# Kernel tuning notes

Measured on AMD Instinct MI355X. Metric: run time of the kernel, lower is better.

## Reference

```python
import jax, jax.numpy as jnp
import numpy as np
from jax import lax

CH, GROUP = 32, 8  # channel=32, subchannel=4 -> group=8

def conv2d(x, w, b, pad):
    # x: [B,C,H,W], w: [O,I,kh,kw]
    out = lax.conv_general_dilated(x, w, (1, 1), [(pad, pad), (pad, pad)],
                                   dimension_numbers=("NCHW", "OIHW", "NCHW"))
    return out + b[None, :, None, None]

def pconv(x, w, b):
    # 1x1 conv as einsum; w: [O,I]
    return jnp.einsum("oi,bihw->bohw", w, x) + b[None, :, None, None]

def setup_inputs() -> dict:
    key = jax.random.key(0)
    ks = jax.random.split(key, 32)
    s = 0.05
    d = {
        "x": jax.random.normal(ks[0], (8, CH, 64, 64), jnp.float32),
        "y": jax.random.normal(ks[1], (8, 1, 64, 64), jnp.float32),
        "conv_w": jax.random.normal(ks[2], (CH, CH + GROUP, 3, 3), jnp.float32) * s,
        "conv_b": jax.random.normal(ks[3], (CH,), jnp.float32) * s,
        "score_w": jax.random.normal(ks[4], (1, CH, 3, 3), jnp.float32) * s,
        "score_b": jax.random.normal(ks[5], (1,), jnp.float32) * s,
        "c132_w": jax.random.normal(ks[6], (32, 1, 3, 3), jnp.float32) * s,
        "c132_b": jax.random.normal(ks[7], (32,), jnp.float32) * s,
        "q1_w": jax.random.normal(ks[8], (32, 32), jnp.float32) * s,
        "q1_b": jax.random.normal(ks[9], (32,), jnp.float32) * s,
        "k1_w": jax.random.normal(ks[10], (32, 32), jnp.float32) * s,
        "k1_b": jax.random.normal(ks[11], (32,), jnp.float32) * s,
        "q2_w": jax.random.normal(ks[12], (32, 32), jnp.float32) * s,
        "q2_b": jax.random.normal(ks[13], (32,), jnp.float32) * s,
        "k2_w": jax.random.normal(ks[14], (32, 32), jnp.float32) * s,
        "k2_b": jax.random.normal(ks[15], (32,), jnp.float32) * s,
        "q3_w": jax.random.normal(ks[16], (32, 32), jnp.float32) * s,
        "q3_b": jax.random.normal(ks[17], (32,), jnp.float32) * s,
        "k3_w": jax.random.normal(ks[18], (32, 32), jnp.float32) * s,
        "k3_b": jax.random.normal(ks[19], (32,), jnp.float32) * s,
        "conv6_w": jax.random.normal(ks[20], (32, 64), jnp.float32) * s,
        "conv6_b": jax.random.normal(ks[21], (32,), jnp.float32) * s,
    }
    return d

def reference(x, y, conv_w, conv_b, score_w, score_b, c132_w, c132_b,
              q1_w, q1_b, k1_w, k1_b, q2_w, q2_b, k2_w, k2_b,
              q3_w, q3_b, k3_w, k3_b, conv6_w, conv6_b):
    B, C, H, W = x.shape
    sub = C // GROUP
    # group-wise chunk + interleave y: [x_g0, y, x_g1, y, ...]
    xg = x.reshape(B, GROUP, sub, H, W)
    yb = jnp.broadcast_to(y[:, None], (B, GROUP, 1, H, W))
    x_cat = jnp.concatenate([xg, yb], axis=2).reshape(B, C + GROUP, H, W)
    x1_co = jax.nn.relu(conv2d(x_cat, conv_w, conv_b, 1))        # [B,32,H,W]
    x2_co = conv2d(y, c132_w, c132_b, 1)                          # [B,32,H,W]

    HW = H * W
    x_query1 = pconv(x1_co, q1_w, q1_b).reshape(B, 32, HW)
    x_key1 = pconv(x1_co, k1_w, k1_b).reshape(B, 32, HW)
    x_query2 = pconv(x1_co, q2_w, q2_b).reshape(B, 32, HW)
    x_key2 = pconv(x1_co, k2_w, k2_b).reshape(B, 32, HW)
    y_query = pconv(x2_co, q3_w, q3_b).reshape(B, 32, HW)
    y_key = pconv(x2_co, k3_w, k3_b).reshape(B, 32, HW)

    # spatial attention [B, HW, HW]
    x_hw = jax.nn.softmax(jnp.einsum("bcn,bcm->bnm", x_query1, x_key2), axis=-1)
    # channel attention [B, 32, 32]
    x_c = jax.nn.softmax(jnp.einsum("bcn,bdn->bcd", x_key1, x_query2), axis=-1)

    xy_hw = jnp.einsum("bcn,bnm->bcm", y_query, x_hw).reshape(B, 32, H, W)
    xy_c = jnp.einsum("bcd,bcn->bdn", x_c, y_key).reshape(B, 32, H, W)

    out_final = pconv(jnp.concatenate([xy_hw, xy_c], axis=1), conv6_w, conv6_b)
    x_out = x + out_final
    y_out = y + conv2d(x_out, score_w, score_b, 1)
    return (x_out, y_out)
```

## Files before the change

kernel.cpp:

```cpp
#include <hip/hip_runtime.h>
#include <hip/hip_bf16.h>
#include <math.h>

#define HW 4096

typedef short bf16x8_t __attribute__((ext_vector_type(8)));
typedef float f32x16_t __attribute__((ext_vector_type(16)));
typedef unsigned int u32;
typedef unsigned int u32x4_t __attribute__((ext_vector_type(4)));
typedef int i32x2_t __attribute__((ext_vector_type(2)));

union castu { u32x4_t u; bf16x8_t s; };

static __device__ __forceinline__ unsigned short f2bf(float f){
    union { __bf16 b; unsigned short u; } c; c.b = (__bf16)f; return c.u;
}
static __device__ __forceinline__ u32 pk2(float lo, float hi){
    return ((u32)f2bf(hi) << 16) | (u32)f2bf(lo);
}
static __device__ __forceinline__ bf16x8_t ldb(const unsigned short* p){
    return *reinterpret_cast<const bf16x8_t*>(p);
}
static __device__ __forceinline__ bf16x8_t ld_xs(const unsigned short* p){
    uint2 lo = *(const uint2*)(p);
    uint2 hi = *(const uint2*)(p + 4);
    castu c; c.u = (u32x4_t){lo.x, lo.y, hi.x, hi.y};
    return c.s;
}
static __device__ __forceinline__ f32x16_t mfma32(bf16x8_t a, bf16x8_t b, f32x16_t c){
    return __builtin_amdgcn_mfma_f32_32x32x16_bf16(a, b, c, 0, 0, 0);
}

#define EXP2_MAG  8388608.0f
#define EXP2_BIAS 1064986816.0f

static __device__ __forceinline__ float fexp2(float x){
    return __int_as_float((int)fmaf(x, EXP2_MAG, EXP2_BIAS));
}
static __device__ __forceinline__ u32 pkexp2(float lo, float hi){
    u32 i0 = (u32)(int)fmaf(lo, EXP2_MAG, EXP2_BIAS);
    u32 i1 = (u32)(int)fmaf(hi, EXP2_MAG, EXP2_BIAS);
#if __has_builtin(__builtin_amdgcn_perm)
    return __builtin_amdgcn_perm(i1, i0, 0x07060302u);
#else
    return (i1 & 0xFFFF0000u) | (i0 >> 16);
#endif
}

static __device__ __forceinline__ void cd2bfrag(const u32 P[8], bf16x8_t& b0, bf16x8_t& b1){
    i32x2_t s02 = __builtin_amdgcn_permlane32_swap((int)P[0], (int)P[2], false, false);
    i32x2_t s13 = __builtin_amdgcn_permlane32_swap((int)P[1], (int)P[3], false, false);
    i32x2_t s46 = __builtin_amdgcn_permlane32_swap((int)P[4], (int)P[6], false, false);
    i32x2_t s57 = __builtin_amdgcn_permlane32_swap((int)P[5], (int)P[7], false, false);
    castu c0, c1;
    c0.u = (u32x4_t){ (u32)s02[0], (u32)s13[0], (u32)s02[1], (u32)s13[1] };
    c1.u = (u32x4_t){ (u32)s46[0], (u32)s57[0], (u32)s46[1], (u32)s57[1] };
    b0 = c0.s; b1 = c1.s;
}

#define LOG2E 1.44269504088896340736f


__global__ __launch_bounds__(256, 1) void k_front_mfma(
    const float* __restrict__ x, const float* __restrict__ y,
    const float* __restrict__ conv_w, const float* __restrict__ conv_b,
    const float* __restrict__ c132_w, const float* __restrict__ c132_b,
    const float* __restrict__ q1w, const float* __restrict__ q1b,
    const float* __restrict__ k1w, const float* __restrict__ k1b,
    const float* __restrict__ q2w, const float* __restrict__ q2b,
    const float* __restrict__ k2w, const float* __restrict__ k2b,
    const float* __restrict__ q3w, const float* __restrict__ q3b,
    const float* __restrict__ k3w, const float* __restrict__ k3b,
    float* __restrict__ K1, float* __restrict__ Q2, float* __restrict__ YQ,
    unsigned short* __restrict__ Q1t, unsigned short* __restrict__ K2t,
    unsigned short* __restrict__ YKt)
{
    __shared__ unsigned short xs[4 * 68 * 36];
    __shared__ float ys[4 * 68];
    __shared__ u32 wplane[18 * 4 * 64];
    __shared__ u32 wyplane[4 * 64];
    __shared__ u32 c1plane[4 * 64];

    int tid = threadIdx.x;
    int h0 = blockIdx.x * 2, b = blockIdx.y;

    #pragma unroll
    for (int i = 0; i < 32; ++i){
        int idx = i * 256 + tid;
        int w = idx & 63, ic = (idx >> 6) & 31, dr = idx >> 11;
        int hr = h0 - 1 + dr;
        float v = (hr >= 0 && hr < 64) ? x[((b * 32 + ic) << 12) + (hr << 6) + w] : 0.f;
        xs[(dr * 68 + w + 1) * 36 + ic] = f2bf(v);
    }
    {
        int dr = tid >> 6, ic = tid & 31, side = (tid >> 5) & 1;
        xs[(dr * 68 + (side ? 65 : 0)) * 36 + ic] = 0;
    }
    for (int idx = tid; idx < 272; idx += 256){
        int dr = idx / 68, wp = idx % 68;
        int hr = h0 - 1 + dr, w = wp - 1;
        ys[idx] = (hr >= 0 && hr < 64 && w >= 0 && w < 64) ? y[(b << 12) + (hr << 6) + w] : 0.f;
    }
    for (int e = tid; e < 4608; e += 256){
        int f = e >> 8, wi = (e >> 6) & 3, ln = e & 63;
        int t = f >> 1, j = f & 1, hh = ln >> 5, ll = ln & 31;
        int ic0 = 16 * j + 8 * hh + 2 * wi;
        int co0 = 5 * (ic0 >> 2) + (ic0 & 3);
        int ic1 = ic0 + 1;
        int co1 = 5 * (ic1 >> 2) + (ic1 & 3);
        wplane[e] = pk2(conv_w[ll * 360 + co0 * 9 + t], conv_w[ll * 360 + co1 * 9 + t]);
    }
    {
        int wi = tid >> 6, ln = tid & 63, hh = ln >> 5, ll = ln & 31;
        u32 vy = 0, vc = 0;
        if (hh == 0){
            int t0 = 2 * wi, t1 = 2 * wi + 1;
            float s0 = 0.f, s1 = 0.f;
            #pragma unroll
            for (int g = 0; g < 8; ++g){
                s0 += conv_w[ll * 360 + (5 * g + 4) * 9 + t0];
                s1 += conv_w[ll * 360 + (5 * g + 4) * 9 + t1];
            }
            vy = pk2(s0, s1);
            vc = pk2(c132_w[ll * 9 + t0], c132_w[ll * 9 + t1]);
        } else if (wi == 0){
            float s0 = 0.f;
            #pragma unroll
            for (int g = 0; g < 8; ++g) s0 += conv_w[ll * 360 + (5 * g + 4) * 9 + 8];
            vy = pk2(s0, 0.f);
            vc = pk2(c132_w[ll * 9 + 8], 0.f);
        }
        wyplane[wi * 64 + ln] = vy;
        c1plane[wi * 64 + ln] = vc;
    }
    __syncthreads();

    int lane = tid & 63, wid = tid >> 6;
    int l31 = lane & 31, h = lane >> 5;
    int wr = wid >> 1, toff = (wid & 1) * 32;
    int wpB = toff + l31;

    bf16x8_t wA[18];
    #pragma unroll
    for (int f = 0; f < 18; ++f){
        castu c;
        c.u = (u32x4_t){ wplane[(f * 4 + 0) * 64 + lane], wplane[(f * 4 + 1) * 64 + lane],
                         wplane[(f * 4 + 2) * 64 + lane], wplane[(f * 4 + 3) * 64 + lane] };
        wA[f] = c.s;
    }
    castu wyf, c1f;
    wyf.u = (u32x4_t){ wyplane[lane], wyplane[64 + lane], wyplane[128 + lane], wyplane[192 + lane] };
    c1f.u = (u32x4_t){ c1plane[lane], c1plane[64 + lane], c1plane[128 + lane], c1plane[192 + lane] };

    float yv[8];
    #pragma unroll
    for (int i = 0; i < 8; ++i){
        int tt = 8 * h + i;
        yv[i] = (tt < 9) ? ys[(wr + tt / 3) * 68 + wpB + (tt % 3)] : 0.f;
    }
    castu yf;
    yf.u = (u32x4_t){ pk2(yv[0], yv[1]), pk2(yv[2], yv[3]), pk2(yv[4], yv[5]), pk2(yv[6], yv[7]) };

    f32x16_t accE, accO, accY, acc2;
    #pragma unroll
    for (int r = 0; r < 16; ++r){
        int oc = (r & 3) + 8 * (r >> 2) + 4 * h;
        accE[r] = 0.f; accO[r] = 0.f;
        accY[r] = conv_b[oc]; acc2[r] = c132_b[oc];
    }
    #pragma unroll
    for (int t = 0; t < 9; ++t){
        int base = ((wr + t / 3) * 68 + wpB + (t % 3)) * 36 + 8 * h;
        bf16x8_t b0 = ld_xs(xs + base);
        bf16x8_t b1 = ld_xs(xs + base + 16);
        if (t & 1){
            accO = mfma32(wA[t * 2 + 0], b0, accO);
            accO = mfma32(wA[t * 2 + 1], b1, accO);
        } else {
            accE = mfma32(wA[t * 2 + 0], b0, accE);
            accE = mfma32(wA[t * 2 + 1], b1, accE);
        }
    }
    accY = mfma32(wyf.s, yf.s, accY);
    acc2 = mfma32(c1f.s, yf.s, acc2);

    f32x16_t x1v;
    #pragma unroll
    for (int r = 0; r < 16; ++r){
        float v = accE[r] + accO[r] + accY[r];
        x1v[r] = v > 0.f ? v : 0.f;
    }
    u32 P[8];
    bf16x8_t x1b0, x1b1, x2b0, x2b1;
    #pragma unroll
    for (int t2 = 0; t2 < 8; ++t2) P[t2] = pk2(x1v[2 * t2], x1v[2 * t2 + 1]);
    cd2bfrag(P, x1b0, x1b1);
    #pragma unroll
    for (int t2 = 0; t2 < 8; ++t2) P[t2] = pk2(acc2[2 * t2], acc2[2 * t2 + 1]);
    cd2bfrag(P, x2b0, x2b1);

    int pxg = (h0 + wr) * 64 + toff + l31;
    int tile = ((h0 + wr) << 1) + (wid & 1);
    size_t tb = ((size_t)b * 128 + tile) * 1024;

    {
        f32x16_t a;
        #pragma unroll
        for (int r = 0; r < 16; ++r) a[r] = q1b[(r & 3) + 8 * (r >> 2) + 4 * h];
        const float* p0 = q1w + l31 * 32 + 8 * h;
        castu w0, w1;
        w0.u = (u32x4_t){ pk2(p0[0],p0[1]), pk2(p0[2],p0[3]), pk2(p0[4],p0[5]), pk2(p0[6],p0[7]) };
        w1.u = (u32x4_t){ pk2(p0[16],p0[17]), pk2(p0[18],p0[19]), pk2(p0[20],p0[21]), pk2(p0[22],p0[23]) };
        a = mfma32(w0.s, x1b0, a);
        a = mfma32(w1.s, x1b1, a);
        u32 Q[8];
        #pragma unroll
        for (int t2 = 0; t2 < 8; ++t2) Q[t2] = pk2(a[2 * t2] * LOG2E, a[2 * t2 + 1] * LOG2E);
        bf16x8_t f0, f1; cd2bfrag(Q, f0, f1);
        *(bf16x8_t*)(Q1t + tb + lane * 8)       = f0;
        *(bf16x8_t*)(Q1t + tb + 512 + lane * 8) = f1;
    }
    {
        f32x16_t a;
        #pragma unroll
        for (int r = 0; r < 16; ++r) a[r] = k1b[(r & 3) + 8 * (r >> 2) + 4 * h];
        const float* p0 = k1w + l31 * 32 + 8 * h;
        castu w0, w1;
        w0.u = (u32x4_t){ pk2(p0[0],p0[1]), pk2(p0[2],p0[3]), pk2(p0[4],p0[5]), pk2(p0[6],p0[7]) };
        w1.u = (u32x4_t){ pk2(p0[16],p0[17]), pk2(p0[18],p0[19]), pk2(p0[20],p0[21]), pk2(p0[22],p0[23]) };
        a = mfma32(w0.s, x1b0, a);
        a = mfma32(w1.s, x1b1, a);
        #pragma unroll
        for (int r = 0; r < 16; ++r)
            K1[(b * 32 + (r & 3) + 8 * (r >> 2) + 4 * h) * HW + pxg] = a[r];
    }
    {
        f32x16_t a;
        #pragma unroll
        for (int r = 0; r < 16; ++r) a[r] = q2b[(r & 3) + 8 * (r >> 2) + 4 * h];
        const float* p0 = q2w + l31 * 32 + 8 * h;
        castu w0, w1;
        w0.u = (u32x4_t){ pk2(p0[0],p0[1]), pk2(p0[2],p0[3]), pk2(p0[4],p0[5]), pk2(p0[6],p0[7]) };
        w1.u = (u32x4_t){ pk2(p0[16],p0[17]), pk2(p0[18],p0[19]), pk2(p0[20],p0[21]), pk2(p0[22],p0[23]) };
        a = mfma32(w0.s, x1b0, a);
        a = mfma32(w1.s, x1b1, a);
        #pragma unroll
        for (int r = 0; r < 16; ++r)
            Q2[(b * 32 + (r & 3) + 8 * (r >> 2) + 4 * h) * HW + pxg] = a[r];
    }
    {
        f32x16_t a;
        #pragma unroll
        for (int r = 0; r < 16; ++r) a[r] = k2b[(r & 3) + 8 * (r >> 2) + 4 * h];
        const float* p0 = k2w + l31 * 32 + 8 * h;
        castu w0, w1;
        w0.u = (u32x4_t){ pk2(p0[0],p0[1]), pk2(p0[2],p0[3]), pk2(p0[4],p0[5]), pk2(p0[6],p0[7]) };
        w1.u = (u32x4_t){ pk2(p0[16],p0[17]), pk2(p0[18],p0[19]), pk2(p0[20],p0[21]), pk2(p0[22],p0[23]) };
        a = mfma32(w0.s, x1b0, a);
        a = mfma32(w1.s, x1b1, a);
        u32 Q[8];
        #pragma unroll
        for (int t2 = 0; t2 < 8; ++t2) Q[t2] = pk2(a[2 * t2], a[2 * t2 + 1]);
        bf16x8_t f0, f1; cd2bfrag(Q, f0, f1);
        *(bf16x8_t*)(K2t + tb + lane * 8)       = f0;
        *(bf16x8_t*)(K2t + tb + 512 + lane * 8) = f1;
    }
    {
        f32x16_t a;
        #pragma unroll
        for (int r = 0; r < 16; ++r) a[r] = q3b[(r & 3) + 8 * (r >> 2) + 4 * h];
        const float* p0 = q3w + l31 * 32 + 8 * h;
        castu w0, w1;
        w0.u = (u32x4_t){ pk2(p0[0],p0[1]), pk2(p0[2],p0[3]), pk2(p0[4],p0[5]), pk2(p0[6],p0[7]) };
        w1.u = (u32x4_t){ pk2(p0[16],p0[17]), pk2(p0[18],p0[19]), pk2(p0[20],p0[21]), pk2(p0[22],p0[23]) };
        a = mfma32(w0.s, x2b0, a);
        a = mfma32(w1.s, x2b1, a);
        #pragma unroll
        for (int r = 0; r < 16; ++r)
            YQ[(b * 32 + (r & 3) + 8 * (r >> 2) + 4 * h) * HW + pxg] = a[r];
    }
    {
        f32x16_t a;
        #pragma unroll
        for (int r = 0; r < 16; ++r) a[r] = k3b[(r & 3) + 8 * (r >> 2) + 4 * h];
        const float* p0 = k3w + l31 * 32 + 8 * h;
        castu w0, w1;
        w0.u = (u32x4_t){ pk2(p0[0],p0[1]), pk2(p0[2],p0[3]), pk2(p0[4],p0[5]), pk2(p0[6],p0[7]) };
        w1.u = (u32x4_t){ pk2(p0[16],p0[17]), pk2(p0[18],p0[19]), pk2(p0[20],p0[21]), pk2(p0[22],p0[23]) };
        a = mfma32(w0.s, x2b0, a);
        a = mfma32(w1.s, x2b1, a);
        u32 Q[8];
        #pragma unroll
        for (int t2 = 0; t2 < 8; ++t2) Q[t2] = pk2(a[2 * t2], a[2 * t2 + 1]);
        bf16x8_t f0, f1; cd2bfrag(Q, f0, f1);
        *(bf16x8_t*)(YKt + tb + lane * 8)       = f0;
        *(bf16x8_t*)(YKt + tb + 512 + lane * 8) = f1;
    }
}

__global__ __launch_bounds__(256) void k_chan_part(
    const float* __restrict__ K1, const float* __restrict__ Q2,
    float* __restrict__ Scp)
{
    __shared__ float k1s[128 * 33];
    __shared__ float q2s[128 * 33];
    int b = blockIdx.x & 7;
    int chunk = blockIdx.x >> 3;
    int n0 = chunk * 128;
    int t = threadIdx.x;
    for (int i = 0; i < 16; ++i){
        int idx = i * 256 + t;
        int c = idx >> 7, nl = idx & 127;
        k1s[nl * 33 + c] = K1[(b * 32 + c) * HW + n0 + nl];
        q2s[nl * 33 + c] = Q2[(b * 32 + c) * HW + n0 + nl];
    }
    __syncthreads();
    float acc[4] = {0.f, 0.f, 0.f, 0.f};
    int d = t & 31, c0 = t >> 5;
    for (int nl = 0; nl < 128; ++nl){
        float qv = q2s[nl * 33 + d];
        #pragma unroll
        for (int i = 0; i < 4; ++i)
            acc[i] = fmaf(k1s[nl * 33 + c0 + 8 * i], qv, acc[i]);
    }
    #pragma unroll
    for (int i = 0; i < 4; ++i)
        Scp[(b * 32 + chunk) * 1024 + (c0 + 8 * i) * 32 + d] = acc[i];
}

__global__ __launch_bounds__(1024) void k_chan_fin(
    const float* __restrict__ Scp, const float* __restrict__ c6w,
    float* __restrict__ M2)
{
    __shared__ float pc[32 * 33];
    int b = blockIdx.x;
    int t = threadIdx.x;
    int c = t >> 5, d = t & 31;
    float s = 0.f;
    for (int k = 0; k < 32; ++k) s += Scp[(b * 32 + k) * 1024 + t];
    float mx = s;
    #pragma unroll
    for (int off = 16; off >= 1; off >>= 1) mx = fmaxf(mx, __shfl_xor(mx, off));
    float e = __expf(s - mx);
    float sum = e;
    #pragma unroll
    for (int off = 16; off >= 1; off >>= 1) sum += __shfl_xor(sum, off);
    pc[c * 33 + d] = e / sum;
    __syncthreads();
    int o = t >> 5, cc = t & 31;
    float m2 = 0.f;
    #pragma unroll
    for (int dd = 0; dd < 32; ++dd)
        m2 = fmaf(c6w[o * 64 + 32 + dd], pc[cc * 33 + dd], m2);
    M2[b * 1024 + o * 32 + cc] = m2;
}

__global__ __launch_bounds__(256, 4) void k_stats_mfma(
    const unsigned short* __restrict__ Q1t, const unsigned short* __restrict__ K2t,
    const float* __restrict__ YQ, unsigned short* __restrict__ YQ2)
{
    __shared__ float red[4][16][64];
    __shared__ float ls[32];
    int t = threadIdx.x, wid = t >> 6, lane = t & 63;
    int l31 = lane & 31, h = lane >> 5;
    int b = blockIdx.x & 7, ntile = blockIdx.x >> 3;
    int n0 = ntile * 32;
    size_t qtb = ((size_t)b * 128 + ntile) * 1024;
    bf16x8_t a0 = ldb(Q1t + qtb + lane * 8);
    bf16x8_t a1 = ldb(Q1t + qtb + 512 + lane * 8);
    float accl[16];
    #pragma unroll
    for (int r = 0; r < 16; ++r) accl[r] = 0.f;

    const unsigned short* kp = K2t + ((size_t)b * 128 + (wid << 5)) * 1024 + lane * 8;
    bf16x8_t b0 = ldb(kp), b1 = ldb(kp + 512);
    f32x16_t s_cur;
    #pragma unroll
    for (int r = 0; r < 16; ++r) s_cur[r] = 0.f;
    s_cur = mfma32(a0, b0, s_cur);
    s_cur = mfma32(a1, b1, s_cur);
    kp += 1024;
    bf16x8_t b0n = ldb(kp), b1n = ldb(kp + 512);

    #pragma unroll 4
    for (int i = 0; i < 32; ++i){
        f32x16_t s_nxt;
        #pragma unroll
        for (int r = 0; r < 16; ++r) s_nxt[r] = 0.f;
        __builtin_amdgcn_s_setprio(1);
        s_nxt = mfma32(a0, b0n, s_nxt);
        s_nxt = mfma32(a1, b1n, s_nxt);
        __builtin_amdgcn_s_setprio(0);
        kp += (i < 30) ? 1024 : 0;
        bf16x8_t b0nn = ldb(kp), b1nn = ldb(kp + 512);
        #pragma unroll
        for (int r = 0; r < 16; ++r) accl[r] += fexp2(s_cur[r]);
        s_cur = s_nxt; b0n = b0nn; b1n = b1nn;
    }
    #pragma unroll
    for (int r = 0; r < 16; ++r) red[wid][r][lane] = accl[r];
    __syncthreads();
    if (wid == 0){
        #pragma unroll
        for (int r = 0; r < 16; ++r){
            float v = red[0][r][lane] + red[1][r][lane] + red[2][r][lane] + red[3][r][lane];
            #pragma unroll
            for (int off = 16; off >= 1; off >>= 1) v += __shfl_xor(v, off);
            if (l31 == 0)
                ls[(r & 3) + 8 * (r >> 2) + 4 * h] = 1.0f / v;
        }
    }
    __syncthreads();
    size_t otb = ((size_t)b * 128 + ntile) * 1024;
    #pragma unroll
    for (int p = 0; p < 4; ++p){
        int idx = (p << 8) + t;
        int c = idx >> 5, n = idx & 31;
        size_t g = (size_t)(b * 32 + c) * HW + n0 + n;
        int j = n >> 4, hh = (n >> 3) & 1;
        YQ2[otb + j * 512 + (c + (hh << 5)) * 8 + (n & 7)] = f2bf(YQ[g] * ls[n]);
    }
}

__global__ __launch_bounds__(256, 4) void k_attn_mfma(
    const unsigned short* __restrict__ Q1t, const unsigned short* __restrict__ K2t,
    const unsigned short* __restrict__ YKt, const unsigned short* __restrict__ YQ2,
    const float* __restrict__ M2, const float* __restrict__ c6w, const float* __restrict__ c6b,
    const float* __restrict__ x, float* __restrict__ xout)
{
    __shared__ float red[4][16][64];
    int t = threadIdx.x, wid = t >> 6, lane = t & 63;
    int l31 = lane & 31, h = lane >> 5;
    int b = blockIdx.x & 7, mtile = blockIdx.x >> 3;
    int m0 = mtile * 32;
    size_t ktb = ((size_t)b * 128 + mtile) * 1024;

    bf16x8_t kb0 = ldb(K2t + ktb + lane * 8);
    bf16x8_t kb1 = ldb(K2t + ktb + 512 + lane * 8);

    f32x16_t oacc;
    #pragma unroll
    for (int r = 0; r < 16; ++r) oacc[r] = 0.f;

    const unsigned short* qp = Q1t + ((size_t)b * 128 + (wid << 5)) * 1024 + lane * 8;
    const unsigned short* yp = YQ2 + ((size_t)b * 128 + (wid << 5)) * 1024 + lane * 8;

    bf16x8_t a0 = ldb(qp), a1 = ldb(qp + 512);
    bf16x8_t y0 = ldb(yp), y1 = ldb(yp + 512);
    f32x16_t s_cur;
    #pragma unroll
    for (int r = 0; r < 16; ++r) s_cur[r] = 0.f;
    s_cur = mfma32(a0, kb0, s_cur);
    s_cur = mfma32(a1, kb1, s_cur);
    qp += 1024; yp += 1024;
    bf16x8_t a0n = ldb(qp), a1n = ldb(qp + 512);
    bf16x8_t y0n = ldb(yp), y1n = ldb(yp + 512);

    #pragma unroll 4
    for (int i = 0; i < 32; ++i){
        f32x16_t s_nxt;
        #pragma unroll
        for (int r = 0; r < 16; ++r) s_nxt[r] = 0.f;
        __builtin_amdgcn_s_setprio(1);
        s_nxt = mfma32(a0n, kb0, s_nxt);
        s_nxt = mfma32(a1n, kb1, s_nxt);
        __builtin_amdgcn_s_setprio(0);
        int adv = (i < 30) ? 1024 : 0;
        qp += adv; yp += adv;
        bf16x8_t a0nn = ldb(qp), a1nn = ldb(qp + 512);
        bf16x8_t y0nn = ldb(yp), y1nn = ldb(yp + 512);
        u32 P[8];
        #pragma unroll
        for (int tt = 0; tt < 8; ++tt)
            P[tt] = pkexp2(s_cur[2 * tt], s_cur[2 * tt + 1]);
        bf16x8_t e0, e1;
        cd2bfrag(P, e0, e1);
        __builtin_amdgcn_s_setprio(1);
        oacc = mfma32(y0, e0, oacc);
        oacc = mfma32(y1, e1, oacc);
        __builtin_amdgcn_s_setprio(0);
        s_cur = s_nxt;
        a0n = a0nn; a1n = a1nn;
        y0 = y0n; y1 = y1n; y0n = y0nn; y1n = y1nn;
    }
    #pragma unroll
    for (int r = 0; r < 16; ++r) red[wid][r][lane] = oacc[r];
    __syncthreads();
    if (wid != 0) return;
    #pragma unroll
    for (int r = 0; r < 16; ++r)
        oacc[r] = red[0][r][lane] + red[1][r][lane] + red[2][r][lane] + red[3][r][lane];

    u32 P[8];
    #pragma unroll
    for (int tt = 0; tt < 8; ++tt) P[tt] = pk2(oacc[2 * tt], oacc[2 * tt + 1]);
    bf16x8_t xb0, xb1;
    cd2bfrag(P, xb0, xb1);

    const float* w1p = c6w + l31 * 64;
    const float* m2p = M2 + b * 1024 + l31 * 32;
    int cb0 = 8 * h, cb1 = 16 + 8 * h;
    castu wa0, wa1, ma0, ma1;
    wa0.u = (u32x4_t){ pk2(w1p[cb0], w1p[cb0+1]), pk2(w1p[cb0+2], w1p[cb0+3]),
                       pk2(w1p[cb0+4], w1p[cb0+5]), pk2(w1p[cb0+6], w1p[cb0+7]) };
    wa1.u = (u32x4_t){ pk2(w1p[cb1], w1p[cb1+1]), pk2(w1p[cb1+2], w1p[cb1+3]),
                       pk2(w1p[cb1+4], w1p[cb1+5]), pk2(w1p[cb1+6], w1p[cb1+7]) };
    ma0.u = (u32x4_t){ pk2(m2p[cb0], m2p[cb0+1]), pk2(m2p[cb0+2], m2p[cb0+3]),
                       pk2(m2p[cb0+4], m2p[cb0+5]), pk2(m2p[cb0+6], m2p[cb0+7]) };
    ma1.u = (u32x4_t){ pk2(m2p[cb1], m2p[cb1+1]), pk2(m2p[cb1+2], m2p[cb1+3]),
                       pk2(m2p[cb1+4], m2p[cb1+5]), pk2(m2p[cb1+6], m2p[cb1+7]) };
    bf16x8_t ykb0 = ldb(YKt + ktb + lane * 8);
    bf16x8_t ykb1 = ldb(YKt + ktb + 512 + lane * 8);

    f32x16_t facc;
    #pragma unroll
    for (int r = 0; r < 16; ++r) facc[r] = c6b[(r & 3) + 8 * (r >> 2) + 4 * h];
    facc = mfma32(wa0.s, xb0, facc);
    facc = mfma32(wa1.s, xb1, facc);
    facc = mfma32(ma0.s, ykb0, facc);
    facc = mfma32(ma1.s, ykb1, facc);

    #pragma unroll
    for (int r = 0; r < 16; ++r){
        int o = (r & 3) + 8 * (r >> 2) + 4 * h;
        size_t gi = ((size_t)(b * 32 + o) << 12) + m0 + l31;
        xout[gi] = x[gi] + facc[r];
    }
}

__global__ __launch_bounds__(256) void k_score(
    const float* __restrict__ xout, const float* __restrict__ y,
    const float* __restrict__ sw, const float* __restrict__ sb,
    float* __restrict__ yout)
{
    __shared__ float xs[3][32][66];
    __shared__ float red[4][64];
    int tid = threadIdx.x;
    int b = blockIdx.x & 7, h = blockIdx.x >> 3;
    for (int i = 0; i < 24; ++i){
        int idx = i * 256 + tid;
        int w = idx & 63, ic = (idx >> 6) & 31, dr = idx >> 11;
        int hr = h + dr - 1;
        xs[dr][ic][1 + w] = (hr >= 0 && hr < 64) ? xout[((b * 32 + ic) << 12) + (hr << 6) + w] : 0.f;
    }
    if (tid < 96){ xs[tid >> 5][tid & 31][0] = 0.f; }
    else if (tid < 192){ int u = tid - 96; xs[u >> 5][u & 31][65] = 0.f; }
    __syncthreads();
    int w = tid & 63, icg = tid >> 6;
    float p = 0.f;
    #pragma unroll
    for (int i = 0; i < 8; ++i){
        int ic = icg * 8 + i;
        #pragma unroll
        for (int tap = 0; tap < 9; ++tap)
            p = fmaf(sw[ic * 9 + tap], xs[tap / 3][ic][w + tap % 3], p);
    }
    red[icg][w] = p;
    __syncthreads();
    if (tid < 64){
        int px = (h << 6) + tid;
        yout[b * HW + px] = y[b * HW + px] + sb[0]
                          + red[0][tid] + red[1][tid] + red[2][tid] + red[3][tid];
    }
}

extern "C" void kernel_launch(void* const* d_in, const int* in_sizes, int n_in,
                              void* d_out, int out_size, void* d_ws, size_t ws_size,
                              hipStream_t stream)
{
    (void)in_sizes; (void)n_in; (void)out_size; (void)ws_size;
    const float* x      = (const float*)d_in[0];
    const float* y      = (const float*)d_in[1];
    const float* conv_w = (const float*)d_in[2];
    const float* conv_b = (const float*)d_in[3];
    const float* score_w= (const float*)d_in[4];
    const float* score_b= (const float*)d_in[5];
    const float* c132_w = (const float*)d_in[6];
    const float* c132_b = (const float*)d_in[7];
    const float* q1w = (const float*)d_in[8];  const float* q1b = (const float*)d_in[9];
    const float* k1w = (const float*)d_in[10]; const float* k1b = (const float*)d_in[11];
    const float* q2w = (const float*)d_in[12]; const float* q2b = (const float*)d_in[13];
    const float* k2w = (const float*)d_in[14]; const float* k2b = (const float*)d_in[15];
    const float* q3w = (const float*)d_in[16]; const float* q3b = (const float*)d_in[17];
    const float* k3w = (const float*)d_in[18]; const float* k3b = (const float*)d_in[19];
    const float* c6w = (const float*)d_in[20]; const float* c6b = (const float*)d_in[21];

    float* ws = (float*)d_ws;
    const size_t SZ = 1048576;
    float* Scp = ws;
    float* M2  = ws + 262144;
    float* K1  = ws + 2 * SZ;
    float* Q2  = ws + 3 * SZ;
    float* YQf = ws + 4 * SZ;
    unsigned short* Q1t = (unsigned short*)(ws + 5 * SZ);
    unsigned short* K2t = (unsigned short*)(ws + 5 * SZ + SZ / 2);
    unsigned short* YKt = (unsigned short*)(ws + 6 * SZ);
    unsigned short* YQ2 = (unsigned short*)(ws + 6 * SZ + SZ / 2);

    float* xout = (float*)d_out;
    float* yout = xout + SZ;

    k_front_mfma<<<dim3(32, 8), 256, 0, stream>>>(
        x, y, conv_w, conv_b, c132_w, c132_b,
        q1w, q1b, k1w, k1b, q2w, q2b, k2w, k2b, q3w, q3b, k3w, k3b,
        K1, Q2, YQf, Q1t, K2t, YKt);
    k_chan_part<<<256, 256, 0, stream>>>(K1, Q2, Scp);
    k_chan_fin<<<8, 1024, 0, stream>>>(Scp, c6w, M2);
    k_stats_mfma<<<1024, 256, 0, stream>>>(Q1t, K2t, YQf, YQ2);
    k_attn_mfma<<<1024, 256, 0, stream>>>(Q1t, K2t, YKt, YQ2, M2, c6w, c6b, x, xout);
    k_score<<<512, 256, 0, stream>>>(xout, y, score_w, score_b, yout);
}
```

Before: 95.29 us.

## Split attention and stats kernels over key halves with separate reduce/epilogue kernels

Splits the softmax-denominator and attention-output kernels along the reduction dimension into two halves, doubling grid size. Partial sums go to workspace buffers and are combined in new k_scale and k_epi kernels, which take over the normalization and output epilogue. The channel-attention partial kernel also uses smaller chunks and twice as many blocks. The aim is more parallelism to fill the GPU, at the cost of extra launches, extra global traffic for partials, and dropping the setprio hints.

Measured after the change: 98.78 us. 3.7% more time.

```diff
diff --git a/kernel.cpp b/kernel.cpp
--- a/kernel.cpp
+++ b/kernel.cpp
@@ -302,22 +302,22 @@
     const float* __restrict__ K1, const float* __restrict__ Q2,
     float* __restrict__ Scp)
 {
-    __shared__ float k1s[128 * 33];
-    __shared__ float q2s[128 * 33];
+    __shared__ float k1s[64 * 33];
+    __shared__ float q2s[64 * 33];
     int b = blockIdx.x & 7;
     int chunk = blockIdx.x >> 3;
-    int n0 = chunk * 128;
+    int n0 = chunk * 64;
     int t = threadIdx.x;
-    for (int i = 0; i < 16; ++i){
+    for (int i = 0; i < 8; ++i){
         int idx = i * 256 + t;
-        int c = idx >> 7, nl = idx & 127;
+        int c = idx >> 6, nl = idx & 63;
         k1s[nl * 33 + c] = K1[(b * 32 + c) * HW + n0 + nl];
         q2s[nl * 33 + c] = Q2[(b * 32 + c) * HW + n0 + nl];
     }
     __syncthreads();
     float acc[4] = {0.f, 0.f, 0.f, 0.f};
     int d = t & 31, c0 = t >> 5;
-    for (int nl = 0; nl < 128; ++nl){
+    for (int nl = 0; nl < 64; ++nl){
         float qv = q2s[nl * 33 + d];
         #pragma unroll
         for (int i = 0; i < 4; ++i)
@@ -325,7 +325,7 @@
     }
     #pragma unroll
     for (int i = 0; i < 4; ++i)
-        Scp[(b * 32 + chunk) * 1024 + (c0 + 8 * i) * 32 + d] = acc[i];
+        Scp[(b * 64 + chunk) * 1024 + (c0 + 8 * i) * 32 + d] = acc[i];
 }
 
 __global__ __launch_bounds__(1024) void k_chan_fin(
@@ -337,7 +337,7 @@
     int t = threadIdx.x;
     int c = t >> 5, d = t & 31;
     float s = 0.f;
-    for (int k = 0; k < 32; ++k) s += Scp[(b * 32 + k) * 1024 + t];
+    for (int k = 0; k < 64; ++k) s += Scp[(b * 64 + k) * 1024 + t];
     float mx = s;
     #pragma unroll
     for (int off = 16; off >= 1; off >>= 1) mx = fmaxf(mx, __shfl_xor(mx, off));
@@ -355,15 +355,16 @@
     M2[b * 1024 + o * 32 + cc] = m2;
 }
 
-__global__ __launch_bounds__(256, 4) void k_stats_mfma(
+__global__ __launch_bounds__(256, 2) void k_stats_mfma(
     const unsigned short* __restrict__ Q1t, const unsigned short* __restrict__ K2t,
-    const float* __restrict__ YQ, unsigned short* __restrict__ YQ2)
+    float* __restrict__ lpart)
 {
     __shared__ float red[4][16][64];
-    __shared__ float ls[32];
     int t = threadIdx.x, wid = t >> 6, lane = t & 63;
     int l31 = lane & 31, h = lane >> 5;
-    int b = blockIdx.x & 7, ntile = blockIdx.x >> 3;
+    int b = blockIdx.x & 7;
+    int ntile = (blockIdx.x >> 3) & 127;
+    int mhalf = blockIdx.x >> 10;
     int n0 = ntile * 32;
     size_t qtb = ((size_t)b * 128 + ntile) * 1024;
     bf16x8_t a0 = ldb(Q1t + qtb + lane * 8);
@@ -371,27 +372,22 @@
     float accl[16];
     #pragma unroll
     for (int r = 0; r < 16; ++r) accl[r] = 0.f;
-
-    const unsigned short* kp = K2t + ((size_t)b * 128 + (wid << 5)) * 1024 + lane * 8;
+    f32x16_t zz;
+    #pragma unroll
+    for (int r = 0; r < 16; ++r) zz[r] = 0.f;
+
+    const unsigned short* kp = K2t + ((size_t)b * 128 + mhalf * 64 + (wid << 4)) * 1024 + lane * 8;
     bf16x8_t b0 = ldb(kp), b1 = ldb(kp + 512);
-    f32x16_t s_cur;
-    #pragma unroll
-    for (int r = 0; r < 16; ++r) s_cur[r] = 0.f;
-    s_cur = mfma32(a0, b0, s_cur);
+    f32x16_t s_cur = mfma32(a0, b0, zz);
     s_cur = mfma32(a1, b1, s_cur);
     kp += 1024;
     bf16x8_t b0n = ldb(kp), b1n = ldb(kp + 512);
 
     #pragma unroll 4
-    for (int i = 0; i < 32; ++i){
-        f32x16_t s_nxt;
-        #pragma unroll
-        for (int r = 0; r < 16; ++r) s_nxt[r] = 0.f;
-        __builtin_amdgcn_s_setprio(1);
-        s_nxt = mfma32(a0, b0n, s_nxt);
+    for (int i = 0; i < 16; ++i){
+        f32x16_t s_nxt = mfma32(a0, b0n, zz);
         s_nxt = mfma32(a1, b1n, s_nxt);
-        __builtin_amdgcn_s_setprio(0);
-        kp += (i < 30) ? 1024 : 0;
+        kp += (i < 14) ? 1024 : 0;
         bf16x8_t b0nn = ldb(kp), b1nn = ldb(kp + 512);
         #pragma unroll
         for (int r = 0; r < 16; ++r) accl[r] += fexp2(s_cur[r]);
@@ -400,15 +396,28 @@
     #pragma unroll
     for (int r = 0; r < 16; ++r) red[wid][r][lane] = accl[r];
     __syncthreads();
-    if (wid == 0){
-        #pragma unroll
-        for (int r = 0; r < 16; ++r){
-            float v = red[0][r][lane] + red[1][r][lane] + red[2][r][lane] + red[3][r][lane];
-            #pragma unroll
-            for (int off = 16; off >= 1; off >>= 1) v += __shfl_xor(v, off);
-            if (l31 == 0)
-                ls[(r & 3) + 8 * (r >> 2) + 4 * h] = 1.0f / v;
-        }
+    if (wid != 0) return;
+    #pragma unroll
+    for (int r = 0; r < 16; ++r){
+        float v = red[0][r][lane] + red[1][r][lane] + red[2][r][lane] + red[3][r][lane];
+        #pragma unroll
+        for (int off = 16; off >= 1; off >>= 1) v += __shfl_xor(v, off);
+        if (l31 == 0)
+            lpart[(size_t)mhalf * 32768 + b * 4096 + n0 + (r & 3) + 8 * (r >> 2) + 4 * h] = v;
+    }
+}
+
+__global__ __launch_bounds__(256) void k_scale(
+    const float* __restrict__ YQ, const float* __restrict__ lpart,
+    unsigned short* __restrict__ YQ2)
+{
+    __shared__ float ls[32];
+    int t = threadIdx.x;
+    int b = blockIdx.x & 7, ntile = blockIdx.x >> 3;
+    int n0 = ntile * 32;
+    if (t < 32){
+        float l = lpart[b * 4096 + n0 + t] + lpart[32768 + b * 4096 + n0 + t];
+        ls[t] = 1.0f / l;
     }
     __syncthreads();
     size_t otb = ((size_t)b * 128 + ntile) * 1024;
@@ -422,50 +431,41 @@
     }
 }
 
-__global__ __launch_bounds__(256, 4) void k_attn_mfma(
+__global__ __launch_bounds__(256, 2) void k_attn_mfma(
     const unsigned short* __restrict__ Q1t, const unsigned short* __restrict__ K2t,
-    const unsigned short* __restrict__ YKt, const unsigned short* __restrict__ YQ2,
-    const float* __restrict__ M2, const float* __restrict__ c6w, const float* __restrict__ c6b,
-    const float* __restrict__ x, float* __restrict__ xout)
+    const unsigned short* __restrict__ YQ2, float* __restrict__ Opart)
 {
     __shared__ float red[4][16][64];
     int t = threadIdx.x, wid = t >> 6, lane = t & 63;
-    int l31 = lane & 31, h = lane >> 5;
-    int b = blockIdx.x & 7, mtile = blockIdx.x >> 3;
-    int m0 = mtile * 32;
+    int b = blockIdx.x & 7;
+    int mtile = (blockIdx.x >> 3) & 127;
+    int nhalf = blockIdx.x >> 10;
     size_t ktb = ((size_t)b * 128 + mtile) * 1024;
 
     bf16x8_t kb0 = ldb(K2t + ktb + lane * 8);
     bf16x8_t kb1 = ldb(K2t + ktb + 512 + lane * 8);
 
-    f32x16_t oacc;
-    #pragma unroll
-    for (int r = 0; r < 16; ++r) oacc[r] = 0.f;
-
-    const unsigned short* qp = Q1t + ((size_t)b * 128 + (wid << 5)) * 1024 + lane * 8;
-    const unsigned short* yp = YQ2 + ((size_t)b * 128 + (wid << 5)) * 1024 + lane * 8;
+    f32x16_t oacc, zz;
+    #pragma unroll
+    for (int r = 0; r < 16; ++r){ oacc[r] = 0.f; zz[r] = 0.f; }
+
+    size_t nbase = (size_t)b * 128 + nhalf * 64 + (wid << 4);
+    const unsigned short* qp = Q1t + nbase * 1024 + lane * 8;
+    const unsigned short* yp = YQ2 + nbase * 1024 + lane * 8;
 
     bf16x8_t a0 = ldb(qp), a1 = ldb(qp + 512);
     bf16x8_t y0 = ldb(yp), y1 = ldb(yp + 512);
-    f32x16_t s_cur;
-    #pragma unroll
-    for (int r = 0; r < 16; ++r) s_cur[r] = 0.f;
-    s_cur = mfma32(a0, kb0, s_cur);
+    f32x16_t s_cur = mfma32(a0, kb0, zz);
     s_cur = mfma32(a1, kb1, s_cur);
     qp += 1024; yp += 1024;
     bf16x8_t a0n = ldb(qp), a1n = ldb(qp + 512);
     bf16x8_t y0n = ldb(yp), y1n = ldb(yp + 512);
 
     #pragma unroll 4
-    for (int i = 0; i < 32; ++i){
-        f32x16_t s_nxt;
-        #pragma unroll
-        for (int r = 0; r < 16; ++r) s_nxt[r] = 0.f;
-        __builtin_amdgcn_s_setprio(1);
-        s_nxt = mfma32(a0n, kb0, s_nxt);
+    for (int i = 0; i < 16; ++i){
+        f32x16_t s_nxt = mfma32(a0n, kb0, zz);
         s_nxt = mfma32(a1n, kb1, s_nxt);
-        __builtin_amdgcn_s_setprio(0);
-        int adv = (i < 30) ? 1024 : 0;
+        int adv = (i < 14) ? 1024 : 0;
         qp += adv; yp += adv;
         bf16x8_t a0nn = ldb(qp), a1nn = ldb(qp + 512);
         bf16x8_t y0nn = ldb(yp), y1nn = ldb(yp + 512);
@@ -487,9 +487,30 @@
     for (int r = 0; r < 16; ++r) red[wid][r][lane] = oacc[r];
     __syncthreads();
     if (wid != 0) return;
+    float* op = Opart + (((size_t)nhalf * 8 + b) * 128 + mtile) * 1024;
     #pragma unroll
     for (int r = 0; r < 16; ++r)
-        oacc[r] = red[0][r][lane] + red[1][r][lane] + red[2][r][lane] + red[3][r][lane];
+        op[r * 64 + lane] = red[0][r][lane] + red[1][r][lane] + red[2][r][lane] + red[3][r][lane];
+}
+
+__global__ __launch_bounds__(256) void k_epi(
+    const float* __restrict__ Opart, const unsigned short* __restrict__ YKt,
+    const float* __restrict__ M2, const float* __restrict__ c6w, const float* __restrict__ c6b,
+    const float* __restrict__ x, float* __restrict__ xout)
+{
+    int t = threadIdx.x, wid = t >> 6, lane = t & 63;
+    int l31 = lane & 31, h = lane >> 5;
+    int b = blockIdx.x & 7;
+    int mtile = (blockIdx.x >> 3) * 4 + wid;
+    int m0 = mtile * 32;
+    size_t ktb = ((size_t)b * 128 + mtile) * 1024;
+
+    const float* p0h = Opart + ((size_t)b * 128 + mtile) * 1024;
+    const float* p1h = Opart + (((size_t)8 + b) * 128 + mtile) * 1024;
+    f32x16_t oacc;
+    #pragma unroll
+    for (int r = 0; r < 16; ++r)
+        oacc[r] = p0h[r * 64 + lane] + p1h[r * 64 + lane];
 
     u32 P[8];
     #pragma unroll
@@ -588,7 +609,7 @@
     float* ws = (float*)d_ws;
     const size_t SZ = 1048576;
     float* Scp = ws;
-    float* M2  = ws + 262144;
+    float* M2  = ws + 524288;
     float* K1  = ws + 2 * SZ;
     float* Q2  = ws + 3 * SZ;
     float* YQf = ws + 4 * SZ;
@@ -596,6 +617,8 @@
     unsigned short* K2t = (unsigned short*)(ws + 5 * SZ + SZ / 2);
     unsigned short* YKt = (unsigned short*)(ws + 6 * SZ);
     unsigned short* YQ2 = (unsigned short*)(ws + 6 * SZ + SZ / 2);
+    float* lpart = ws + 7 * SZ;
+    float* Opart = ws + 8 * SZ;
 
     float* xout = (float*)d_out;
     float* yout = xout + SZ;
@@ -604,9 +627,11 @@
         x, y, conv_w, conv_b, c132_w, c132_b,
         q1w, q1b, k1w, k1b, q2w, q2b, k2w, k2b, q3w, q3b, k3w, k3b,
         K1, Q2, YQf, Q1t, K2t, YKt);
-    k_chan_part<<<256, 256, 0, stream>>>(K1, Q2, Scp);
+    k_chan_part<<<512, 256, 0, stream>>>(K1, Q2, Scp);
     k_chan_fin<<<8, 1024, 0, stream>>>(Scp, c6w, M2);
-    k_stats_mfma<<<1024, 256, 0, stream>>>(Q1t, K2t, YQf, YQ2);
-    k_attn_mfma<<<1024, 256, 0, stream>>>(Q1t, K2t, YKt, YQ2, M2, c6w, c6b, x, xout);
+    k_stats_mfma<<<2048, 256, 0, stream>>>(Q1t, K2t, lpart);
+    k_scale<<<1024, 256, 0, stream>>>(YQf, lpart, YQ2);
+    k_attn_mfma<<<2048, 256, 0, stream>>>(Q1t, K2t, YQ2, Opart);
+    k_epi<<<256, 256, 0, stream>>>(Opart, YKt, M2, c6w, c6b, x, xout);
     k_score<<<512, 256, 0, stream>>>(xout, y, score_w, score_b, yout);
 }
```

## Process two query/key tiles per block in attention kernels and split channel partials finer

Applied to the files above, without the earlier changes.

The stats and attention kernels now each handle two 32-wide tiles per block, so every streamed K2/Q1/YQ2 fragment is reused for two MFMA score computations. This halves the grid and the global fragment traffic per output tile. The software-pipelined score prefetch and its priority hints are dropped, and launch bounds go from 4 to 2 blocks per CU to make room for the extra registers, which may cost latency hiding. Separately, the channel-partial kernel uses 64-column chunks over 512 blocks, and the finalize kernel sums 64 partials, with the M2 buffer moved to match.

Measured after the change: 91.92 us. -3.5%, faster.

```diff
diff --git a/kernel.cpp b/kernel.cpp
--- a/kernel.cpp
+++ b/kernel.cpp
@@ -302,22 +302,22 @@
     const float* __restrict__ K1, const float* __restrict__ Q2,
     float* __restrict__ Scp)
 {
-    __shared__ float k1s[128 * 33];
-    __shared__ float q2s[128 * 33];
+    __shared__ float k1s[64 * 33];
+    __shared__ float q2s[64 * 33];
     int b = blockIdx.x & 7;
     int chunk = blockIdx.x >> 3;
-    int n0 = chunk * 128;
+    int n0 = chunk * 64;
     int t = threadIdx.x;
-    for (int i = 0; i < 16; ++i){
+    for (int i = 0; i < 8; ++i){
         int idx = i * 256 + t;
-        int c = idx >> 7, nl = idx & 127;
+        int c = idx >> 6, nl = idx & 63;
         k1s[nl * 33 + c] = K1[(b * 32 + c) * HW + n0 + nl];
         q2s[nl * 33 + c] = Q2[(b * 32 + c) * HW + n0 + nl];
     }
     __syncthreads();
     float acc[4] = {0.f, 0.f, 0.f, 0.f};
     int d = t & 31, c0 = t >> 5;
-    for (int nl = 0; nl < 128; ++nl){
+    for (int nl = 0; nl < 64; ++nl){
         float qv = q2s[nl * 33 + d];
         #pragma unroll
         for (int i = 0; i < 4; ++i)
@@ -325,7 +325,7 @@
     }
     #pragma unroll
     for (int i = 0; i < 4; ++i)
-        Scp[(b * 32 + chunk) * 1024 + (c0 + 8 * i) * 32 + d] = acc[i];
+        Scp[(b * 64 + chunk) * 1024 + (c0 + 8 * i) * 32 + d] = acc[i];
 }
 
 __global__ __launch_bounds__(1024) void k_chan_fin(
@@ -337,7 +337,7 @@
     int t = threadIdx.x;
     int c = t >> 5, d = t & 31;
     float s = 0.f;
-    for (int k = 0; k < 32; ++k) s += Scp[(b * 32 + k) * 1024 + t];
+    for (int k = 0; k < 64; ++k) s += Scp[(b * 64 + k) * 1024 + t];
     float mx = s;
     #pragma unroll
     for (int off = 16; off >= 1; off >>= 1) mx = fmaxf(mx, __shfl_xor(mx, off));
@@ -355,116 +355,118 @@
     M2[b * 1024 + o * 32 + cc] = m2;
 }
 
-__global__ __launch_bounds__(256, 4) void k_stats_mfma(
+__global__ __launch_bounds__(256, 2) void k_stats_mfma(
     const unsigned short* __restrict__ Q1t, const unsigned short* __restrict__ K2t,
     const float* __restrict__ YQ, unsigned short* __restrict__ YQ2)
 {
-    __shared__ float red[4][16][64];
-    __shared__ float ls[32];
+    __shared__ float redA[4][16][64];
+    __shared__ float redB[4][16][64];
+    __shared__ float ls[64];
     int t = threadIdx.x, wid = t >> 6, lane = t & 63;
     int l31 = lane & 31, h = lane >> 5;
-    int b = blockIdx.x & 7, ntile = blockIdx.x >> 3;
-    int n0 = ntile * 32;
-    size_t qtb = ((size_t)b * 128 + ntile) * 1024;
-    bf16x8_t a0 = ldb(Q1t + qtb + lane * 8);
-    bf16x8_t a1 = ldb(Q1t + qtb + 512 + lane * 8);
-    float accl[16];
-    #pragma unroll
-    for (int r = 0; r < 16; ++r) accl[r] = 0.f;
+    int b = blockIdx.x & 7, npair = blockIdx.x >> 3;
+    int nA = npair * 2;
+    size_t qtbA = ((size_t)b * 128 + nA) * 1024;
+    bf16x8_t aA0 = ldb(Q1t + qtbA + lane * 8);
+    bf16x8_t aA1 = ldb(Q1t + qtbA + 512 + lane * 8);
+    bf16x8_t aB0 = ldb(Q1t + qtbA + 1024 + lane * 8);
+    bf16x8_t aB1 = ldb(Q1t + qtbA + 1536 + lane * 8);
+    float acclA[16], acclB[16];
+    #pragma unroll
+    for (int r = 0; r < 16; ++r){ acclA[r] = 0.f; acclB[r] = 0.f; }
+    f32x16_t zz;
+    #pragma unroll
+    for (int r = 0; r < 16; ++r) zz[r] = 0.f;
 
     const unsigned short* kp = K2t + ((size_t)b * 128 + (wid << 5)) * 1024 + lane * 8;
     bf16x8_t b0 = ldb(kp), b1 = ldb(kp + 512);
-    f32x16_t s_cur;
-    #pragma unroll
-    for (int r = 0; r < 16; ++r) s_cur[r] = 0.f;
-    s_cur = mfma32(a0, b0, s_cur);
-    s_cur = mfma32(a1, b1, s_cur);
     kp += 1024;
     bf16x8_t b0n = ldb(kp), b1n = ldb(kp + 512);
 
-    #pragma unroll 4
+    #pragma unroll 2
     for (int i = 0; i < 32; ++i){
-        f32x16_t s_nxt;
-        #pragma unroll
-        for (int r = 0; r < 16; ++r) s_nxt[r] = 0.f;
-        __builtin_amdgcn_s_setprio(1);
-        s_nxt = mfma32(a0, b0n, s_nxt);
-        s_nxt = mfma32(a1, b1n, s_nxt);
-        __builtin_amdgcn_s_setprio(0);
+        f32x16_t sA = mfma32(aA0, b0, zz);
+        sA = mfma32(aA1, b1, sA);
+        f32x16_t sB = mfma32(aB0, b0, zz);
+        sB = mfma32(aB1, b1, sB);
         kp += (i < 30) ? 1024 : 0;
         bf16x8_t b0nn = ldb(kp), b1nn = ldb(kp + 512);
         #pragma unroll
-        for (int r = 0; r < 16; ++r) accl[r] += fexp2(s_cur[r]);
-        s_cur = s_nxt; b0n = b0nn; b1n = b1nn;
-    }
-    #pragma unroll
-    for (int r = 0; r < 16; ++r) red[wid][r][lane] = accl[r];
-    __syncthreads();
-    if (wid == 0){
+        for (int r = 0; r < 16; ++r) acclA[r] += fexp2(sA[r]);
+        #pragma unroll
+        for (int r = 0; r < 16; ++r) acclB[r] += fexp2(sB[r]);
+        b0 = b0n; b1 = b1n; b0n = b0nn; b1n = b1nn;
+    }
+    #pragma unroll
+    for (int r = 0; r < 16; ++r){
+        redA[wid][r][lane] = acclA[r];
+        redB[wid][r][lane] = acclB[r];
+    }
+    __syncthreads();
+    if (wid < 2){
+        const float* rp = (wid == 0) ? &redA[0][0][0] : &redB[0][0][0];
         #pragma unroll
         for (int r = 0; r < 16; ++r){
-            float v = red[0][r][lane] + red[1][r][lane] + red[2][r][lane] + red[3][r][lane];
+            float v = rp[r * 64 + lane] + rp[1024 + r * 64 + lane]
+                    + rp[2048 + r * 64 + lane] + rp[3072 + r * 64 + lane];
             #pragma unroll
             for (int off = 16; off >= 1; off >>= 1) v += __shfl_xor(v, off);
             if (l31 == 0)
-                ls[(r & 3) + 8 * (r >> 2) + 4 * h] = 1.0f / v;
+                ls[wid * 32 + (r & 3) + 8 * (r >> 2) + 4 * h] = 1.0f / v;
         }
     }
     __syncthreads();
-    size_t otb = ((size_t)b * 128 + ntile) * 1024;
-    #pragma unroll
-    for (int p = 0; p < 4; ++p){
+    #pragma unroll
+    for (int p = 0; p < 8; ++p){
         int idx = (p << 8) + t;
-        int c = idx >> 5, n = idx & 31;
-        size_t g = (size_t)(b * 32 + c) * HW + n0 + n;
+        int tl = idx >> 10;
+        int i1 = idx & 1023;
+        int c = i1 >> 5, n = i1 & 31;
+        size_t g = (size_t)(b * 32 + c) * HW + (nA + tl) * 32 + n;
         int j = n >> 4, hh = (n >> 3) & 1;
-        YQ2[otb + j * 512 + (c + (hh << 5)) * 8 + (n & 7)] = f2bf(YQ[g] * ls[n]);
-    }
-}
-
-__global__ __launch_bounds__(256, 4) void k_attn_mfma(
+        YQ2[((size_t)b * 128 + nA + tl) * 1024 + j * 512 + (c + (hh << 5)) * 8 + (n & 7)]
+            = f2bf(YQ[g] * ls[tl * 32 + n]);
+    }
+}
+
+__global__ __launch_bounds__(256, 2) void k_attn_mfma(
     const unsigned short* __restrict__ Q1t, const unsigned short* __restrict__ K2t,
     const unsigned short* __restrict__ YKt, const unsigned short* __restrict__ YQ2,
     const float* __restrict__ M2, const float* __restrict__ c6w, const float* __restrict__ c6b,
     const float* __restrict__ x, float* __restrict__ xout)
 {
-    __shared__ float red[4][16][64];
+    __shared__ float redA[4][16][64];
+    __shared__ float redB[4][16][64];
     int t = threadIdx.x, wid = t >> 6, lane = t & 63;
     int l31 = lane & 31, h = lane >> 5;
-    int b = blockIdx.x & 7, mtile = blockIdx.x >> 3;
-    int m0 = mtile * 32;
-    size_t ktb = ((size_t)b * 128 + mtile) * 1024;
-
-    bf16x8_t kb0 = ldb(K2t + ktb + lane * 8);
-    bf16x8_t kb1 = ldb(K2t + ktb + 512 + lane * 8);
-
-    f32x16_t oacc;
-    #pragma unroll
-    for (int r = 0; r < 16; ++r) oacc[r] = 0.f;
+    int b = blockIdx.x & 7, mpair = blockIdx.x >> 3;
+    int mA = mpair * 2;
+    size_t ktbA = ((size_t)b * 128 + mA) * 1024;
+
+    bf16x8_t kbA0 = ldb(K2t + ktbA + lane * 8);
+    bf16x8_t kbA1 = ldb(K2t + ktbA + 512 + lane * 8);
+    bf16x8_t kbB0 = ldb(K2t + ktbA + 1024 + lane * 8);
+    bf16x8_t kbB1 = ldb(K2t + ktbA + 1536 + lane * 8);
+
+    f32x16_t oaccA, oaccB, zz;
+    #pragma unroll
+    for (int r = 0; r < 16; ++r){ oaccA[r] = 0.f; oaccB[r] = 0.f; zz[r] = 0.f; }
 
     const unsigned short* qp = Q1t + ((size_t)b * 128 + (wid << 5)) * 1024 + lane * 8;
     const unsigned short* yp = YQ2 + ((size_t)b * 128 + (wid << 5)) * 1024 + lane * 8;
 
     bf16x8_t a0 = ldb(qp), a1 = ldb(qp + 512);
     bf16x8_t y0 = ldb(yp), y1 = ldb(yp + 512);
-    f32x16_t s_cur;
-    #pragma unroll
-    for (int r = 0; r < 16; ++r) s_cur[r] = 0.f;
-    s_cur = mfma32(a0, kb0, s_cur);
-    s_cur = mfma32(a1, kb1, s_cur);
     qp += 1024; yp += 1024;
     bf16x8_t a0n = ldb(qp), a1n = ldb(qp + 512);
     bf16x8_t y0n = ldb(yp), y1n = ldb(yp + 512);
 
-    #pragma unroll 4
+    #pragma unroll 2
     for (int i = 0; i < 32; ++i){
-        f32x16_t s_nxt;
-        #pragma unroll
-        for (int r = 0; r < 16; ++r) s_nxt[r] = 0.f;
-        __builtin_amdgcn_s_setprio(1);
-        s_nxt = mfma32(a0n, kb0, s_nxt);
-        s_nxt = mfma32(a1n, kb1, s_nxt);
-        __builtin_amdgcn_s_setprio(0);
+        f32x16_t sA = mfma32(a0, kbA0, zz);
+        sA = mfma32(a1, kbA1, sA);
+        f32x16_t sB = mfma32(a0, kbB0, zz);
+        sB = mfma32(a1, kbB1, sB);
         int adv = (i < 30) ? 1024 : 0;
         qp += adv; yp += adv;
         bf16x8_t a0nn = ldb(qp), a1nn = ldb(qp + 512);
@@ -472,24 +474,41 @@
         u32 P[8];
         #pragma unroll
         for (int tt = 0; tt < 8; ++tt)
-            P[tt] = pkexp2(s_cur[2 * tt], s_cur[2 * tt + 1]);
+            P[tt] = pkexp2(sA[2 * tt], sA[2 * tt + 1]);
         bf16x8_t e0, e1;
         cd2bfrag(P, e0, e1);
         __builtin_amdgcn_s_setprio(1);
-        oacc = mfma32(y0, e0, oacc);
-        oacc = mfma32(y1, e1, oacc);
+        oaccA = mfma32(y0, e0, oaccA);
+        oaccA = mfma32(y1, e1, oaccA);
         __builtin_amdgcn_s_setprio(0);
-        s_cur = s_nxt;
-        a0n = a0nn; a1n = a1nn;
-        y0 = y0n; y1 = y1n; y0n = y0nn; y1n = y1nn;
-    }
-    #pragma unroll
-    for (int r = 0; r < 16; ++r) red[wid][r][lane] = oacc[r];
-    __syncthreads();
-    if (wid != 0) return;
+        #pragma unroll
+        for (int tt = 0; tt < 8; ++tt)
+            P[tt] = pkexp2(sB[2 * tt], sB[2 * tt + 1]);
+        cd2bfrag(P, e0, e1);
+        __builtin_amdgcn_s_setprio(1);
+        oaccB = mfma32(y0, e0, oaccB);
+        oaccB = mfma32(y1, e1, oaccB);
+        __builtin_amdgcn_s_setprio(0);
+        a0 = a0n; a1 = a1n; y0 = y0n; y1 = y1n;
+        a0n = a0nn; a1n = a1nn; y0n = y0nn; y1n = y1nn;
+    }
+    #pragma unroll
+    for (int r = 0; r < 16; ++r){
+        redA[wid][r][lane] = oaccA[r];
+        redB[wid][r][lane] = oaccB[r];
+    }
+    __syncthreads();
+    if (wid >= 2) return;
+    const float* rp = (wid == 0) ? &redA[0][0][0] : &redB[0][0][0];
+    f32x16_t oacc;
     #pragma unroll
     for (int r = 0; r < 16; ++r)
-        oacc[r] = red[0][r][lane] + red[1][r][lane] + red[2][r][lane] + red[3][r][lane];
+        oacc[r] = rp[r * 64 + lane] + rp[1024 + r * 64 + lane]
+                + rp[2048 + r * 64 + lane] + rp[3072 + r * 64 + lane];
+
+    int mtile = mA + wid;
+    int m0 = mtile * 32;
+    size_t ktb = ((size_t)b * 128 + mtile) * 1024;
 
     u32 P[8];
     #pragma unroll
@@ -588,7 +607,7 @@
     float* ws = (float*)d_ws;
     const size_t SZ = 1048576;
     float* Scp = ws;
-    float* M2  = ws + 262144;
+    float* M2  = ws + 524288;
     float* K1  = ws + 2 * SZ;
     float* Q2  = ws + 3 * SZ;
     float* YQf = ws + 4 * SZ;
@@ -604,9 +623,9 @@
         x, y, conv_w, conv_b, c132_w, c132_b,
         q1w, q1b, k1w, k1b, q2w, q2b, k2w, k2b, q3w, q3b, k3w, k3b,
         K1, Q2, YQf, Q1t, K2t, YKt);
-    k_chan_part<<<256, 256, 0, stream>>>(K1, Q2, Scp);
+    k_chan_part<<<512, 256, 0, stream>>>(K1, Q2, Scp);
     k_chan_fin<<<8, 1024, 0, stream>>>(Scp, c6w, M2);
-    k_stats_mfma<<<1024, 256, 0, stream>>>(Q1t, K2t, YQf, YQ2);
-    k_attn_mfma<<<1024, 256, 0, stream>>>(Q1t, K2t, YKt, YQ2, M2, c6w, c6b, x, xout);
+    k_stats_mfma<<<512, 256, 0, stream>>>(Q1t, K2t, YQf, YQ2);
+    k_attn_mfma<<<512, 256, 0, stream>>>(Q1t, K2t, YKt, YQ2, M2, c6w, c6b, x, xout);
     k_score<<<512, 256, 0, stream>>>(xout, y, score_w, score_b, yout);
 }
```
